# Performance work log

Measured on AMD Instinct MI355X. Metric: run time of the kernel, lower is better.

The kernel has to match this reference:

```python
import jax, jax.numpy as jnp
import numpy as np

NUM_NEIGHBORS = 9  # cfg['num_neighbors']


def _cdist(a, b):
    """Euclidean cdist. a: [..., M, D], b: [..., N, D] -> [..., M, N]."""
    a2 = jnp.sum(a * a, axis=-1)[..., :, None]
    b2 = jnp.sum(b * b, axis=-1)[..., None, :]
    ab = jnp.einsum('...md,...nd->...mn', a, b)
    return jnp.sqrt(jnp.maximum(a2 + b2 - 2.0 * ab, 0.0))


def setup_inputs() -> dict:
    key = jax.random.key(0)
    k1, k2 = jax.random.split(key)
    B, P, D, N = 8, 784, 384, 16384
    embedding = jax.random.normal(k1, (B * P, D), dtype=jnp.float32)
    embedding_coreset = jax.random.normal(k2, (N, D), dtype=jnp.float32)
    return {"embedding": embedding, "embedding_coreset": embedding_coreset, "batch_size": B}


def reference(embedding, embedding_coreset, batch_size):
    D = embedding.shape[-1]
    # 1-NN of every patch against the coreset
    dists = _cdist(embedding, embedding_coreset)          # [B*P, N]
    patch_scores = jnp.min(dists, axis=1).reshape(batch_size, -1)   # [B, P]
    locations = jnp.argmin(dists, axis=1).reshape(batch_size, -1)   # [B, P]

    b = jnp.arange(batch_size)
    max_patches = jnp.argmax(patch_scores, axis=1)        # [B]
    emb = embedding.reshape(batch_size, -1, D)            # [B, P, D]
    max_feats = emb[b, max_patches]                       # [B, D]
    score = patch_scores[b, max_patches]                  # [B]
    nn_index = locations[b, max_patches]                  # [B]
    nn_sample = embedding_coreset[nn_index]               # [B, D]

    # k-NN of the nearest coreset sample within the coreset (support set)
    d_nn = _cdist(nn_sample, embedding_coreset)           # [B, N]
    _, support = jax.lax.top_k(-d_nn, NUM_NEIGHBORS)      # smallest dists, ascending -> [B, K]
    support_feats = embedding_coreset[support]            # [B, K, D]

    # distances from max patch feature to the support samples
    d_sup = _cdist(max_feats[:, None, :], support_feats)[:, 0, :]  # [B, K]
    weights = (1.0 - jax.nn.softmax(d_sup, axis=1))[:, 0]          # [B]
    return weights * score
```

## Files before the change

### kernel.cpp

```cpp
#include <hip/hip_runtime.h>
#include <hip/hip_bf16.h>
#include <math.h>

#define M_TOTAL 6272
#define N_CS    16384
#define D_DIM   384
#define BATCH   8
#define P_PATCH 784
#define KNN     9

#define MTILES  (M_TOTAL / 128)
#define NTILES2 (N_CS / 256)
#define NBLK    (M_TOTAL / 4)
#define PBB     196

typedef _Float16 half8 __attribute__((ext_vector_type(8)));
typedef float    floatx4 __attribute__((ext_vector_type(4)));

__device__ __forceinline__ void async_copy16(const void* g, void* l) {
    __builtin_amdgcn_global_load_lds(
        (const __attribute__((address_space(1))) void*)g,
        (__attribute__((address_space(3))) void*)l, 16, 0, 0);
}

__device__ __forceinline__ unsigned long long shfl_xor_u64(unsigned long long v, int mk) {
    int lo = __shfl_xor((int)(unsigned)v, mk, 64);
    int hi = __shfl_xor((int)(unsigned)(v >> 32), mk, 64);
    return ((unsigned long long)(unsigned)hi << 32) | (unsigned)lo;
}

__global__ void convert_all_kernel(const float* __restrict__ emb,
                                   const float* __restrict__ cs,
                                   _Float16* __restrict__ embh,
                                   _Float16* __restrict__ csh,
                                   float* __restrict__ cnorm) {
    int w = threadIdx.x >> 6, lane = threadIdx.x & 63;
    int row = blockIdx.x * 4 + w;
    if (row >= N_CS + M_TOTAL) return;
    bool is_cs = row < N_CS;
    const float* r = (is_cs ? cs + (size_t)row * D_DIM
                            : emb + (size_t)(row - N_CS) * D_DIM) + lane * 6;
    float2 a = *(const float2*)r;
    float2 b = *(const float2*)(r + 2);
    float2 c = *(const float2*)(r + 4);
    union { _Float16 h[2]; unsigned u; } p0, p1, p2;
    p0.h[0] = (_Float16)a.x; p0.h[1] = (_Float16)a.y;
    p1.h[0] = (_Float16)b.x; p1.h[1] = (_Float16)b.y;
    p2.h[0] = (_Float16)c.x; p2.h[1] = (_Float16)c.y;
    unsigned* dst = (unsigned*)(is_cs ? csh + (size_t)row * D_DIM
                                      : embh + (size_t)(row - N_CS) * D_DIM) + lane * 3;
    dst[0] = p0.u; dst[1] = p1.u; dst[2] = p2.u;
    if (is_cs) {
        float s = a.x * a.x + a.y * a.y + b.x * b.x + b.y * b.y + c.x * c.x + c.y * c.y;
#pragma unroll
        for (int mk = 1; mk <= 32; mk <<= 1) s += __shfl_xor(s, mk, 64);
        if (lane == 0) cnorm[row] = s;
    }
}

__global__ __launch_bounds__(256, 2) void mindist_mfma_kernel(
    const _Float16* __restrict__ embh, const _Float16* __restrict__ csh,
    const float* __restrict__ cnorm,
    float* __restrict__ pvals, int* __restrict__ pidx) {
    __shared__ _Float16 As0[128 * 32];
    __shared__ _Float16 As1[128 * 32];
    __shared__ _Float16 Bs0[256 * 32];
    __shared__ _Float16 Bs1[256 * 32];

    const int b    = blockIdx.x;
    const int bx   = b >> 6;
    const int by   = ((b & 7) << 3) | ((b >> 3) & 7);
    const int tid  = threadIdx.x;
    const int lane = tid & 63;
    const int w    = tid >> 6;
    const int wr   = w >> 1, wc = w & 1;
    const int row0  = bx * 128;
    const int cbase = by * 256;
    const int q   = lane >> 4;
    const int cl  = lane & 15;

    floatx4 acc[4][8];
#pragma unroll
    for (int mi = 0; mi < 4; ++mi)
#pragma unroll
        for (int nj = 0; nj < 8; ++nj) acc[mi][nj] = (floatx4){0.f, 0.f, 0.f, 0.f};

    float cn_l[8];
#pragma unroll
    for (int nj = 0; nj < 8; ++nj)
        cn_l[nj] = cnorm[cbase + wc * 128 + nj * 16 + cl];

    const int sub4 = lane >> 2;
    const int ch   = lane & 3;

#define STAGE(AS, BS, KK)                                                     \
    {                                                                         \
        _Pragma("unroll")                                                     \
        for (int i = 0; i < 6; ++i) {                                         \
            int inst = w * 6 + i;                                             \
            if (inst < 8) {                                                   \
                int r  = inst * 16 + sub4;                                    \
                int sc = (ch ^ ((r >> 1) & 3)) * 8;                           \
                async_copy16(embh + (size_t)(row0 + r) * D_DIM + (KK) + sc,   \
                             &AS[inst * 512 + lane * 8]);                     \
            } else {                                                          \
                int blk = inst - 8;                                           \
                int r   = blk * 16 + sub4;                                    \
                int sc  = (ch ^ ((r >> 1) & 3)) * 8;                          \
                async_copy16(csh + (size_t)(cbase + r) * D_DIM + (KK) + sc,   \
                             &BS[blk * 512 + lane * 8]);                      \
            }                                                                 \
        }                                                                     \
    }

#define COMPUTE(AS, BS)                                                       \
    {                                                                         \
        half8 af[4], bf[8];                                                   \
        _Pragma("unroll")                                                     \
        for (int mi = 0; mi < 4; ++mi) {                                      \
            int R = wr * 64 + mi * 16 + cl;                                   \
            af[mi] = *(const half8*)&AS[R * 32 + ((q ^ ((R >> 1) & 3)) * 8)]; \
        }                                                                     \
        _Pragma("unroll")                                                     \
        for (int nj = 0; nj < 8; ++nj) {                                      \
            int R = wc * 128 + nj * 16 + cl;                                  \
            bf[nj] = *(const half8*)&BS[R * 32 + ((q ^ ((R >> 1) & 3)) * 8)]; \
        }                                                                     \
        _Pragma("unroll")                                                     \
        for (int mi = 0; mi < 4; ++mi)                                        \
            _Pragma("unroll")                                                 \
            for (int nj = 0; nj < 8; ++nj)                                    \
                acc[mi][nj] = __builtin_amdgcn_mfma_f32_16x16x32_f16(         \
                    af[mi], bf[nj], acc[mi][nj], 0, 0, 0);                    \
    }

    STAGE(As0, Bs0, 0);
    int kk = 0;
#pragma unroll 1
    for (int jj = 0; jj < 5; ++jj) {
        __syncthreads();
        STAGE(As1, Bs1, kk + 32);
        COMPUTE(As0, Bs0);
        __syncthreads();
        STAGE(As0, Bs0, kk + 64);
        COMPUTE(As1, Bs1);
        kk += 64;
    }
    __syncthreads();
    STAGE(As1, Bs1, kk + 32);
    COMPUTE(As0, Bs0);
    __syncthreads();
    COMPUTE(As1, Bs1);
#undef STAGE
#undef COMPUTE

    __syncthreads();
    float* smv = (float*)As0;
    int*   smi = (int*)(As0 + 512);

#pragma unroll
    for (int mi = 0; mi < 4; ++mi) {
#pragma unroll
        for (int r = 0; r < 4; ++r) {
            float v = 3.4e38f; int idx = 0x7fffffff;
#pragma unroll
            for (int nj = 0; nj < 8; ++nj) {
                float d = cn_l[nj] - 2.f * acc[mi][nj][r];
                int   c = cbase + wc * 128 + nj * 16 + cl;
                if (d < v) { v = d; idx = c; }
            }
#pragma unroll
            for (int mk = 1; mk <= 8; mk <<= 1) {
                float v2 = __shfl_xor(v, mk, 64);
                int   i2 = __shfl_xor(idx, mk, 64);
                if (v2 < v || (v2 == v && i2 < idx)) { v = v2; idx = i2; }
            }
            if (cl == 0) {
                int rl = wr * 64 + mi * 16 + q * 4 + r;
                smv[rl * 2 + wc] = v;
                smi[rl * 2 + wc] = idx;
            }
        }
    }
    __syncthreads();
    if (tid < 128) {
        float v = smv[tid * 2];      int i = smi[tid * 2];
        float v1 = smv[tid * 2 + 1]; int i1 = smi[tid * 2 + 1];
        if (v1 < v) { v = v1; i = i1; }
        pvals[(size_t)(row0 + tid) * NTILES2 + by] = v;
        pidx[(size_t)(row0 + tid) * NTILES2 + by]  = i;
    }
}

__global__ void reduce_rescore_kernel(const float* __restrict__ pvals,
                                      const int* __restrict__ pidx,
                                      const float* __restrict__ emb,
                                      const float* __restrict__ cs,
                                      int* __restrict__ loc,
                                      unsigned long long* __restrict__ partial) {
    __shared__ unsigned long long keys[4];
    int w = threadIdx.x >> 6, lane = threadIdx.x & 63;
    int m = blockIdx.x * 4 + w;
    float v = pvals[(size_t)m * NTILES2 + lane];
    int   i = pidx[(size_t)m * NTILES2 + lane];
#pragma unroll
    for (int mk = 1; mk <= 32; mk <<= 1) {
        float v2 = __shfl_xor(v, mk, 64);
        int   i2 = __shfl_xor(i, mk, 64);
        if (v2 < v || (v2 == v && i2 < i)) { v = v2; i = i2; }
    }
    const float* a = emb + (size_t)m * D_DIM;
    const float* bp = cs + (size_t)i * D_DIM;
    float s = 0.f;
#pragma unroll
    for (int t = 0; t < D_DIM / 64; ++t) {
        float d = a[lane + t * 64] - bp[lane + t * 64];
        s += d * d;
    }
#pragma unroll
    for (int mk = 1; mk <= 32; mk <<= 1) s += __shfl_xor(s, mk, 64);
    if (lane == 0) {
        float sc = sqrtf(s);
        loc[m] = i;
        int p = m % P_PATCH;
        keys[w] = ((unsigned long long)__float_as_uint(sc) << 32) |
                  (unsigned)(0x7fffffff - p);
    }
    __syncthreads();
    if (threadIdx.x == 0) {
        unsigned long long k = keys[0];
        if (keys[1] > k) k = keys[1];
        if (keys[2] > k) k = keys[2];
        if (keys[3] > k) k = keys[3];
        partial[blockIdx.x] = k;
    }
}

__global__ void dnn_kernel(const float* __restrict__ cs,
                           const float* __restrict__ cnorm,
                           const unsigned long long* __restrict__ partial,
                           const int* __restrict__ loc,
                           float* __restrict__ dmat) {
    __shared__ int bnnS[BATCH];
    {
        int bb = threadIdx.x >> 5, l32 = threadIdx.x & 31;
        unsigned long long best = 0ull;
        for (int j = l32; j < PBB; j += 32) {
            unsigned long long k = partial[bb * PBB + j];
            if (k > best) best = k;
        }
#pragma unroll
        for (int mk = 1; mk <= 16; mk <<= 1) {
            unsigned long long o = shfl_xor_u64(best, mk);
            if (o > best) best = o;
        }
        if (l32 == 0) {
            int p = 0x7fffffff - (unsigned)(best & 0xffffffffull);
            bnnS[bb] = loc[bb * P_PATCH + p];
        }
    }
    __syncthreads();

    int lane = threadIdx.x & 63;
    int gw = (blockIdx.x * 256 + threadIdx.x) >> 6;
    float qv[BATCH][6];
#pragma unroll
    for (int b = 0; b < BATCH; ++b) {
        const float* qr = cs + (size_t)bnnS[b] * D_DIM + lane * 6;
#pragma unroll
        for (int j = 0; j < 6; ++j) qv[b][j] = qr[j];
    }
    for (int n = gw; n < N_CS; n += 1024) {
        const float* r = cs + (size_t)n * D_DIM + lane * 6;
        float x[6];
#pragma unroll
        for (int j = 0; j < 6; ++j) x[j] = r[j];
        float s[BATCH];
#pragma unroll
        for (int b = 0; b < BATCH; ++b) {
            float t = 0.f;
#pragma unroll
            for (int j = 0; j < 6; ++j) t += x[j] * qv[b][j];
            s[b] = t;
        }
#pragma unroll
        for (int b = 0; b < BATCH; ++b)
#pragma unroll
            for (int mk = 1; mk <= 32; mk <<= 1) s[b] += __shfl_xor(s[b], mk, 64);
        if (lane < BATCH) {
            float sv = s[0];
#pragma unroll
            for (int b = 1; b < BATCH; ++b) sv = (lane == b) ? s[b] : sv;
            dmat[(size_t)lane * N_CS + n] = cnorm[n] - 2.f * sv;
        }
    }
}

__device__ inline void merge9(float* av, int* ai, const float* bv, const int* bi) {
    float mv[KNN]; int mi[KNN];
    int x = 0, y = 0;
#pragma unroll
    for (int k = 0; k < KNN; ++k) {
        bool ta = (av[x] < bv[y]) || (av[x] == bv[y] && ai[x] < bi[y]);
        if (ta) { mv[k] = av[x]; mi[k] = ai[x]; ++x; }
        else    { mv[k] = bv[y]; mi[k] = bi[y]; ++y; }
    }
#pragma unroll
    for (int k = 0; k < KNN; ++k) { av[k] = mv[k]; ai[k] = mi[k]; }
}

__global__ void top9_final_kernel(const float* __restrict__ dmat,
                                  const float* __restrict__ emb,
                                  const float* __restrict__ cs,
                                  const unsigned long long* __restrict__ partial,
                                  float* __restrict__ out) {
    int b = blockIdx.x;
    int tid = threadIdx.x;
    __shared__ float lv[512][KNN];
    __shared__ int   li[512][KNN];
    __shared__ float mf[D_DIM];
    __shared__ float dsup[KNN];
    __shared__ float bscoreS;
    __shared__ int   bpatchS;

    if (tid < 64) {
        unsigned long long best = 0ull;
        for (int j = tid; j < PBB; j += 64) {
            unsigned long long k = partial[b * PBB + j];
            if (k > best) best = k;
        }
#pragma unroll
        for (int mk = 1; mk <= 32; mk <<= 1) {
            unsigned long long o = shfl_xor_u64(best, mk);
            if (o > best) best = o;
        }
        if (tid == 0) {
            bpatchS = 0x7fffffff - (unsigned)(best & 0xffffffffull);
            bscoreS = __uint_as_float((unsigned)(best >> 32));
        }
    }
    __syncthreads();
    int mp = bpatchS;
    const float* frow = emb + (size_t)(b * P_PATCH + mp) * D_DIM;
    for (int i = tid; i < D_DIM; i += 512) mf[i] = frow[i];

    float tv[KNN]; int ti[KNN];
#pragma unroll
    for (int k = 0; k < KNN; ++k) { tv[k] = 3.4e38f; ti[k] = 0x7fffffff; }
    for (int n = tid; n < N_CS; n += 512) {
        float d = dmat[(size_t)b * N_CS + n];
        if (d < tv[KNN - 1] || (d == tv[KNN - 1] && n < ti[KNN - 1])) {
            tv[KNN - 1] = d; ti[KNN - 1] = n;
#pragma unroll
            for (int k = KNN - 1; k > 0; --k) {
                if (tv[k] < tv[k - 1] || (tv[k] == tv[k - 1] && ti[k] < ti[k - 1])) {
                    float fv = tv[k]; tv[k] = tv[k - 1]; tv[k - 1] = fv;
                    int   iv = ti[k]; ti[k] = ti[k - 1]; ti[k - 1] = iv;
                }
            }
        }
    }
#pragma unroll
    for (int k = 0; k < KNN; ++k) { lv[tid][k] = tv[k]; li[tid][k] = ti[k]; }
    __syncthreads();
    for (int off = 256; off > 0; off >>= 1) {
        if (tid < off) {
            float av[KNN]; int ai[KNN]; float bv2[KNN]; int bi2[KNN];
#pragma unroll
            for (int k = 0; k < KNN; ++k) {
                av[k]  = lv[tid][k];        ai[k]  = li[tid][k];
                bv2[k] = lv[tid + off][k];  bi2[k] = li[tid + off][k];
            }
            merge9(av, ai, bv2, bi2);
#pragma unroll
            for (int k = 0; k < KNN; ++k) { lv[tid][k] = av[k]; li[tid][k] = ai[k]; }
        }
        __syncthreads();
    }
    {
        int k      = tid >> 5;
        int lane32 = tid & 31;
        if (k < KNN) {
            int idx = li[0][k];
            const float* r = cs + (size_t)idx * D_DIM;
            float s = 0.f;
            for (int i = lane32; i < D_DIM; i += 32) {
                float df = mf[i] - r[i];
                s += df * df;
            }
#pragma unroll
            for (int mk = 1; mk <= 16; mk <<= 1) s += __shfl_xor(s, mk, 64);
            if (lane32 == 0) dsup[k] = sqrtf(fmaxf(s, 0.f));
        }
    }
    __syncthreads();
    if (tid == 0) {
        float mx = dsup[0];
        for (int k = 1; k < KNN; ++k) mx = fmaxf(mx, dsup[k]);
        float sum = 0.f, e0 = 0.f;
        for (int k = 0; k < KNN; ++k) {
            float e = expf(dsup[k] - mx);
            sum += e;
            if (k == 0) e0 = e;
        }
        out[b] = (1.f - e0 / sum) * bscoreS;
    }
}

extern "C" void kernel_launch(void* const* d_in, const int* in_sizes, int n_in,
                              void* d_out, int out_size, void* d_ws, size_t ws_size,
                              hipStream_t stream) {
    (void)in_sizes; (void)n_in; (void)out_size; (void)ws_size;
    const float* emb = (const float*)d_in[0];
    const float* cs  = (const float*)d_in[1];
    float* out = (float*)d_out;

    char* p = (char*)d_ws;
    float* cnorm  = (float*)p;  p += (size_t)N_CS * 4;
    float* pvals  = (float*)p;  p += (size_t)M_TOTAL * NTILES2 * 4;
    int*   pidx   = (int*)p;    p += (size_t)M_TOTAL * NTILES2 * 4;
    int*   loc    = (int*)p;    p += (size_t)M_TOTAL * 4;
    p = (char*)(((size_t)p + 7) & ~(size_t)7);
    unsigned long long* partial = (unsigned long long*)p; p += NBLK * 8;
    float* dmat   = (float*)p;  p += (size_t)BATCH * N_CS * 4;
    p = (char*)(((size_t)p + 15) & ~(size_t)15);
    _Float16* embh = (_Float16*)p; p += (size_t)M_TOTAL * D_DIM * 2;
    _Float16* csh  = (_Float16*)p; p += (size_t)N_CS * D_DIM * 2;

    {
        int rows = N_CS + M_TOTAL;
        convert_all_kernel<<<(rows + 3) / 4, 256, 0, stream>>>(emb, cs, embh, csh, cnorm);
    }
    mindist_mfma_kernel<<<MTILES * NTILES2, 256, 0, stream>>>(embh, csh, cnorm,
                                                              pvals, pidx);
    reduce_rescore_kernel<<<NBLK, 256, 0, stream>>>(pvals, pidx, emb, cs, loc, partial);
    dnn_kernel<<<256, 256, 0, stream>>>(cs, cnorm, partial, loc, dmat);
    top9_final_kernel<<<BATCH, 512, 0, stream>>>(dmat, emb, cs, partial, out);
}
```

Measured before the change: 284.8 us.

## Fuse coreset distance and top-9 selection into sliced partial-kNN kernel

Replaces the kernel that wrote a full batch-by-coreset distance matrix and the single-block-per-batch top-9 scan with a sliced kernel. Each block handles one batch and one coreset slice, computes distances on the fly and keeps a per-wave top-9, then merges. A small final kernel picks the global top-9 from the slice candidates by serial selection. This removes the distance-matrix round trip and the slow 8-block scan, but rereads the coreset once per batch and has fewer threads per query.

```diff
diff --git a/kernel.cpp b/kernel.cpp
--- a/kernel.cpp
+++ b/kernel.cpp
@@ -13,6 +13,8 @@
 #define NTILES2 (N_CS / 256)
 #define NBLK    (M_TOTAL / 4)
 #define PBB     196
+#define KSL     16
+#define KROWS   (N_CS / KSL)
 
 typedef _Float16 half8 __attribute__((ext_vector_type(8)));
 typedef float    floatx4 __attribute__((ext_vector_type(4)));
@@ -236,66 +238,6 @@
     }
 }
 
-__global__ void dnn_kernel(const float* __restrict__ cs,
-                           const float* __restrict__ cnorm,
-                           const unsigned long long* __restrict__ partial,
-                           const int* __restrict__ loc,
-                           float* __restrict__ dmat) {
-    __shared__ int bnnS[BATCH];
-    {
-        int bb = threadIdx.x >> 5, l32 = threadIdx.x & 31;
-        unsigned long long best = 0ull;
-        for (int j = l32; j < PBB; j += 32) {
-            unsigned long long k = partial[bb * PBB + j];
-            if (k > best) best = k;
-        }
-#pragma unroll
-        for (int mk = 1; mk <= 16; mk <<= 1) {
-            unsigned long long o = shfl_xor_u64(best, mk);
-            if (o > best) best = o;
-        }
-        if (l32 == 0) {
-            int p = 0x7fffffff - (unsigned)(best & 0xffffffffull);
-            bnnS[bb] = loc[bb * P_PATCH + p];
-        }
-    }
-    __syncthreads();
-
-    int lane = threadIdx.x & 63;
-    int gw = (blockIdx.x * 256 + threadIdx.x) >> 6;
-    float qv[BATCH][6];
-#pragma unroll
-    for (int b = 0; b < BATCH; ++b) {
-        const float* qr = cs + (size_t)bnnS[b] * D_DIM + lane * 6;
-#pragma unroll
-        for (int j = 0; j < 6; ++j) qv[b][j] = qr[j];
-    }
-    for (int n = gw; n < N_CS; n += 1024) {
-        const float* r = cs + (size_t)n * D_DIM + lane * 6;
-        float x[6];
-#pragma unroll
-        for (int j = 0; j < 6; ++j) x[j] = r[j];
-        float s[BATCH];
-#pragma unroll
-        for (int b = 0; b < BATCH; ++b) {
-            float t = 0.f;
-#pragma unroll
-            for (int j = 0; j < 6; ++j) t += x[j] * qv[b][j];
-            s[b] = t;
-        }
-#pragma unroll
-        for (int b = 0; b < BATCH; ++b)
-#pragma unroll
-            for (int mk = 1; mk <= 32; mk <<= 1) s[b] += __shfl_xor(s[b], mk, 64);
-        if (lane < BATCH) {
-            float sv = s[0];
-#pragma unroll
-            for (int b = 1; b < BATCH; ++b) sv = (lane == b) ? s[b] : sv;
-            dmat[(size_t)lane * N_CS + n] = cnorm[n] - 2.f * sv;
-        }
-    }
-}
-
 __device__ inline void merge9(float* av, int* ai, const float* bv, const int* bi) {
     float mv[KNN]; int mi[KNN];
     int x = 0, y = 0;
@@ -309,16 +251,98 @@
     for (int k = 0; k < KNN; ++k) { av[k] = mv[k]; ai[k] = mi[k]; }
 }
 
-__global__ void top9_final_kernel(const float* __restrict__ dmat,
-                                  const float* __restrict__ emb,
-                                  const float* __restrict__ cs,
-                                  const unsigned long long* __restrict__ partial,
-                                  float* __restrict__ out) {
-    int b = blockIdx.x;
-    int tid = threadIdx.x;
-    __shared__ float lv[512][KNN];
-    __shared__ int   li[512][KNN];
+__global__ void knn_partial_kernel(const float* __restrict__ cs,
+                                   const float* __restrict__ cnorm,
+                                   const unsigned long long* __restrict__ partial,
+                                   const int* __restrict__ loc,
+                                   float* __restrict__ kv, int* __restrict__ ki) {
+    const int blk = blockIdx.x;
+    const int bb  = blk >> 4;
+    const int sl  = blk & 15;
+    const int w = threadIdx.x >> 6, lane = threadIdx.x & 63;
+    __shared__ int bnnS;
+    __shared__ float lvS[4][KNN];
+    __shared__ int   liS[4][KNN];
+
+    if (threadIdx.x < 64) {
+        unsigned long long best = 0ull;
+        for (int j = lane; j < PBB; j += 64) {
+            unsigned long long k = partial[bb * PBB + j];
+            if (k > best) best = k;
+        }
+#pragma unroll
+        for (int mk = 1; mk <= 32; mk <<= 1) {
+            unsigned long long o = shfl_xor_u64(best, mk);
+            if (o > best) best = o;
+        }
+        if (lane == 0) {
+            int p = 0x7fffffff - (unsigned)(best & 0xffffffffull);
+            bnnS = loc[bb * P_PATCH + p];
+        }
+    }
+    __syncthreads();
+
+    float qv[6];
+    {
+        const float* qr = cs + (size_t)bnnS * D_DIM + lane * 6;
+#pragma unroll
+        for (int j = 0; j < 6; ++j) qv[j] = qr[j];
+    }
+
+    float tv[KNN]; int ti[KNN];
+#pragma unroll
+    for (int k = 0; k < KNN; ++k) { tv[k] = 3.4e38f; ti[k] = 0x7fffffff; }
+    const int base = sl * KROWS;
+    for (int j = 0; j < KROWS / 4; ++j) {
+        int n = base + j * 4 + w;
+        const float* r = cs + (size_t)n * D_DIM + lane * 6;
+        float s = r[0] * qv[0] + r[1] * qv[1] + r[2] * qv[2]
+                + r[3] * qv[3] + r[4] * qv[4] + r[5] * qv[5];
+#pragma unroll
+        for (int mk = 1; mk <= 32; mk <<= 1) s += __shfl_xor(s, mk, 64);
+        float d = cnorm[n] - 2.f * s;
+        if (d < tv[KNN - 1] || (d == tv[KNN - 1] && n < ti[KNN - 1])) {
+            tv[KNN - 1] = d; ti[KNN - 1] = n;
+#pragma unroll
+            for (int k = KNN - 1; k > 0; --k) {
+                if (tv[k] < tv[k - 1] || (tv[k] == tv[k - 1] && ti[k] < ti[k - 1])) {
+                    float fv = tv[k]; tv[k] = tv[k - 1]; tv[k - 1] = fv;
+                    int   iv = ti[k]; ti[k] = ti[k - 1]; ti[k - 1] = iv;
+                }
+            }
+        }
+    }
+    if (lane == 0) {
+#pragma unroll
+        for (int k = 0; k < KNN; ++k) { lvS[w][k] = tv[k]; liS[w][k] = ti[k]; }
+    }
+    __syncthreads();
+    if (threadIdx.x == 0) {
+        float av[KNN]; int ai[KNN];
+#pragma unroll
+        for (int k = 0; k < KNN; ++k) { av[k] = lvS[0][k]; ai[k] = liS[0][k]; }
+        for (int ww = 1; ww < 4; ++ww) merge9(av, ai, lvS[ww], liS[ww]);
+#pragma unroll
+        for (int k = 0; k < KNN; ++k) {
+            kv[blk * KNN + k] = av[k];
+            ki[blk * KNN + k] = ai[k];
+        }
+    }
+}
+
+__global__ void knn_final_kernel(const float* __restrict__ kv,
+                                 const int* __restrict__ ki,
+                                 const float* __restrict__ emb,
+                                 const float* __restrict__ cs,
+                                 const unsigned long long* __restrict__ partial,
+                                 float* __restrict__ out) {
+    const int b = blockIdx.x;
+    const int tid = threadIdx.x;
+    const int NCAND = KSL * KNN;
+    __shared__ float cv[NCAND];
+    __shared__ int   ci[NCAND];
     __shared__ float mf[D_DIM];
+    __shared__ int   sel[KNN];
     __shared__ float dsup[KNN];
     __shared__ float bscoreS;
     __shared__ int   bpatchS;
@@ -339,50 +363,31 @@
             bscoreS = __uint_as_float((unsigned)(best >> 32));
         }
     }
-    __syncthreads();
-    int mp = bpatchS;
-    const float* frow = emb + (size_t)(b * P_PATCH + mp) * D_DIM;
+    if (tid < NCAND) {
+        cv[tid] = kv[b * NCAND + tid];
+        ci[tid] = ki[b * NCAND + tid];
+    }
+    __syncthreads();
+    const float* frow = emb + (size_t)(b * P_PATCH + bpatchS) * D_DIM;
     for (int i = tid; i < D_DIM; i += 512) mf[i] = frow[i];
 
-    float tv[KNN]; int ti[KNN];
-#pragma unroll
-    for (int k = 0; k < KNN; ++k) { tv[k] = 3.4e38f; ti[k] = 0x7fffffff; }
-    for (int n = tid; n < N_CS; n += 512) {
-        float d = dmat[(size_t)b * N_CS + n];
-        if (d < tv[KNN - 1] || (d == tv[KNN - 1] && n < ti[KNN - 1])) {
-            tv[KNN - 1] = d; ti[KNN - 1] = n;
-#pragma unroll
-            for (int k = KNN - 1; k > 0; --k) {
-                if (tv[k] < tv[k - 1] || (tv[k] == tv[k - 1] && ti[k] < ti[k - 1])) {
-                    float fv = tv[k]; tv[k] = tv[k - 1]; tv[k - 1] = fv;
-                    int   iv = ti[k]; ti[k] = ti[k - 1]; ti[k - 1] = iv;
+    if (tid == 0) {
+        for (int k = 0; k < KNN; ++k) {
+            float bv = 3.4e38f; int bi = 0x7fffffff; int bj = -1;
+            for (int j = 0; j < NCAND; ++j) {
+                if (cv[j] < bv || (cv[j] == bv && ci[j] < bi)) {
+                    bv = cv[j]; bi = ci[j]; bj = j;
                 }
             }
-        }
-    }
-#pragma unroll
-    for (int k = 0; k < KNN; ++k) { lv[tid][k] = tv[k]; li[tid][k] = ti[k]; }
-    __syncthreads();
-    for (int off = 256; off > 0; off >>= 1) {
-        if (tid < off) {
-            float av[KNN]; int ai[KNN]; float bv2[KNN]; int bi2[KNN];
-#pragma unroll
-            for (int k = 0; k < KNN; ++k) {
-                av[k]  = lv[tid][k];        ai[k]  = li[tid][k];
-                bv2[k] = lv[tid + off][k];  bi2[k] = li[tid + off][k];
-            }
-            merge9(av, ai, bv2, bi2);
-#pragma unroll
-            for (int k = 0; k < KNN; ++k) { lv[tid][k] = av[k]; li[tid][k] = ai[k]; }
-        }
-        __syncthreads();
-    }
+            sel[k] = bi;
+            cv[bj] = 3.4e38f; ci[bj] = 0x7fffffff;
+        }
+    }
+    __syncthreads();
     {
-        int k      = tid >> 5;
-        int lane32 = tid & 31;
+        int k = tid >> 5, lane32 = tid & 31;
         if (k < KNN) {
-            int idx = li[0][k];
-            const float* r = cs + (size_t)idx * D_DIM;
+            const float* r = cs + (size_t)sel[k] * D_DIM;
             float s = 0.f;
             for (int i = lane32; i < D_DIM; i += 32) {
                 float df = mf[i] - r[i];
@@ -422,7 +427,8 @@
     int*   loc    = (int*)p;    p += (size_t)M_TOTAL * 4;
     p = (char*)(((size_t)p + 7) & ~(size_t)7);
     unsigned long long* partial = (unsigned long long*)p; p += NBLK * 8;
-    float* dmat   = (float*)p;  p += (size_t)BATCH * N_CS * 4;
+    float* kv     = (float*)p;  p += BATCH * KSL * KNN * 4;
+    int*   ki     = (int*)p;    p += BATCH * KSL * KNN * 4;
     p = (char*)(((size_t)p + 15) & ~(size_t)15);
     _Float16* embh = (_Float16*)p; p += (size_t)M_TOTAL * D_DIM * 2;
     _Float16* csh  = (_Float16*)p; p += (size_t)N_CS * D_DIM * 2;
@@ -434,6 +440,6 @@
     mindist_mfma_kernel<<<MTILES * NTILES2, 256, 0, stream>>>(embh, csh, cnorm,
                                                               pvals, pidx);
     reduce_rescore_kernel<<<NBLK, 256, 0, stream>>>(pvals, pidx, emb, cs, loc, partial);
-    dnn_kernel<<<256, 256, 0, stream>>>(cs, cnorm, partial, loc, dmat);
-    top9_final_kernel<<<BATCH, 512, 0, stream>>>(dmat, emb, cs, partial, out);
-}
+    knn_partial_kernel<<<BATCH * KSL, 256, 0, stream>>>(cs, cnorm, partial, loc, kv, ki);
+    knn_final_kernel<<<BATCH, 512, 0, stream>>>(kv, ki, emb, cs, partial, out);
+}
```

Result: slower. 449.0 us (+57.6%).
